# Optimization experiments

Hardware: AMD Instinct MI355X
Metric: run time of the kernel (lower is better)

Reference implementation:

```python
import jax, jax.numpy as jnp
import numpy as np

B, LQ, D, H, L, P, DFF = 16, 1024, 256, 8, 4, 4, 1024
SHAPES = ((64, 64), (32, 32), (16, 16), (8, 8))  # (H_l, W_l) per level
LV = sum(h * w for h, w in SHAPES)  # 5440
DH = D // H
EPS = 1e-5


def layer_norm(x, g, b):
    m = jnp.mean(x, -1, keepdims=True)
    v = jnp.mean((x - m) ** 2, -1, keepdims=True)
    return (x - m) * jax.lax.rsqrt(v + EPS) * g + b


def mha(q_in, k_in, v_in, w, b, ow, ob):
    # torch nn.MultiheadAttention with packed in_proj [3D, D]
    q = (q_in @ w[:D].T + b[:D]).reshape(B, LQ, H, DH)
    k = (k_in @ w[D:2 * D].T + b[D:2 * D]).reshape(B, LQ, H, DH)
    v = (v_in @ w[2 * D:].T + b[2 * D:]).reshape(B, LQ, H, DH)
    a = jax.nn.softmax(jnp.einsum('bqhd,bkhd->bhqk', q, k) * (1.0 / np.sqrt(DH)), -1)
    o = jnp.einsum('bhqk,bkhd->bqhd', a, v).reshape(B, LQ, D)
    return o @ ow.T + ob


def ms_deform_attn(q, ref, src, value_w, value_b, off_w, off_b, attw_w, attw_b, outp_w, outp_b):
    # value: [B, H, LV, DH]
    value = (src @ value_w.T + value_b).reshape(B, LV, H, DH).transpose(0, 2, 1, 3)
    off = (q @ off_w.T + off_b).reshape(B, LQ, H, L, P, 2)
    attw = jax.nn.softmax((q @ attw_w.T + attw_b).reshape(B, LQ, H, L * P), -1).reshape(B, LQ, H, L, P)
    # offset normalizer = (W_l, H_l) matching (x, y) order of reference points
    normalizer = jnp.array([[w, h] for h, w in SHAPES], jnp.float32)
    loc = ref[:, :, None, :, None, :] + off / normalizer[None, None, None, :, None, :]  # [B,LQ,H,L,P,2]
    out = jnp.zeros((B, LQ, H, DH), jnp.float32)
    start = 0
    for l, (hl, wl) in enumerate(SHAPES):
        v = value[:, :, start:start + hl * wl]  # [B,H,N_l,DH]
        start += hl * wl
        # grid_sample semantics, align_corners=False, padding zeros
        x = loc[:, :, :, l, :, 0] * wl - 0.5  # [B,LQ,H,P]
        y = loc[:, :, :, l, :, 1] * hl - 0.5
        x0 = jnp.floor(x); y0 = jnp.floor(y)
        lx = (x - x0).transpose(0, 2, 1, 3)[..., None]  # [B,H,LQ,P,1]
        ly = (y - y0).transpose(0, 2, 1, 3)[..., None]
        x0i = x0.astype(jnp.int32); y0i = y0.astype(jnp.int32)

        def gather(xi, yi):
            valid = ((xi >= 0) & (xi < wl) & (yi >= 0) & (yi < hl)).astype(jnp.float32)
            idx = jnp.clip(yi, 0, hl - 1) * wl + jnp.clip(xi, 0, wl - 1)  # [B,LQ,H,P]
            idx2 = idx.transpose(0, 2, 1, 3).reshape(B, H, LQ * P)
            g = jnp.take_along_axis(v, jnp.broadcast_to(idx2[..., None], (B, H, LQ * P, DH)), axis=2)
            return g.reshape(B, H, LQ, P, DH) * valid.transpose(0, 2, 1, 3)[..., None]

        g00 = gather(x0i, y0i); g01 = gather(x0i + 1, y0i)
        g10 = gather(x0i, y0i + 1); g11 = gather(x0i + 1, y0i + 1)
        sampled = (g00 * (1 - lx) * (1 - ly) + g01 * lx * (1 - ly)
                   + g10 * (1 - lx) * ly + g11 * lx * ly)  # [B,H,LQ,P,DH]
        out = out + jnp.einsum('bhqpd,bqhp->bqhd', sampled, attw[:, :, :, l])
    return out.reshape(B, LQ, D) @ outp_w.T + outp_b


def setup_inputs() -> dict:
    key = jax.random.key(0)
    ks = jax.random.split(key, 16)
    s = 0.02
    inp = {}
    inp['tgt'] = jax.random.normal(ks[0], (B, LQ, D), jnp.float32)
    inp['query_pos'] = jax.random.normal(ks[1], (B, LQ, D), jnp.float32)
    inp['reference_points'] = jax.random.uniform(ks[2], (B, LQ, L, 2), jnp.float32)
    inp['src'] = jax.random.normal(ks[3], (B, LV, D), jnp.float32)
    # self-attention (MHA)
    inp['in_proj_w'] = jax.random.normal(ks[4], (3 * D, D), jnp.float32) * s
    inp['in_proj_b'] = jnp.zeros((3 * D,), jnp.float32)
    inp['out_proj_w'] = jax.random.normal(ks[5], (D, D), jnp.float32) * s
    inp['out_proj_b'] = jnp.zeros((D,), jnp.float32)
    inp['norm2_g'] = jnp.ones((D,), jnp.float32); inp['norm2_b'] = jnp.zeros((D,), jnp.float32)
    # MSDeformAttn
    inp['value_w'] = jax.random.normal(ks[6], (D, D), jnp.float32) * s
    inp['value_b'] = jnp.zeros((D,), jnp.float32)
    inp['off_w'] = jax.random.normal(ks[7], (H * L * P * 2, D), jnp.float32) * s
    inp['off_b'] = jax.random.normal(ks[8], (H * L * P * 2,), jnp.float32) * 0.5
    inp['attw_w'] = jax.random.normal(ks[9], (H * L * P, D), jnp.float32) * s
    inp['attw_b'] = jnp.zeros((H * L * P,), jnp.float32)
    inp['outp_w'] = jax.random.normal(ks[10], (D, D), jnp.float32) * s
    inp['outp_b'] = jnp.zeros((D,), jnp.float32)
    inp['norm1_g'] = jnp.ones((D,), jnp.float32); inp['norm1_b'] = jnp.zeros((D,), jnp.float32)
    # FFN
    inp['lin1_w'] = jax.random.normal(ks[11], (DFF, D), jnp.float32) * s
    inp['lin1_b'] = jnp.zeros((DFF,), jnp.float32)
    inp['lin2_w'] = jax.random.normal(ks[12], (D, DFF), jnp.float32) * s
    inp['lin2_b'] = jnp.zeros((D,), jnp.float32)
    inp['norm3_g'] = jnp.ones((D,), jnp.float32); inp['norm3_b'] = jnp.zeros((D,), jnp.float32)
    inp['src_spatial_shapes'] = jnp.array(SHAPES, jnp.int32)
    inp['level_start_index'] = jnp.array(np.concatenate([[0], np.cumsum([h * w for h, w in SHAPES[:-1]])]), jnp.int32)
    return inp


def reference(tgt, query_pos, reference_points, src,
              in_proj_w, in_proj_b, out_proj_w, out_proj_b, norm2_g, norm2_b,
              value_w, value_b, off_w, off_b, attw_w, attw_b, outp_w, outp_b,
              norm1_g, norm1_b, lin1_w, lin1_b, lin2_w, lin2_b, norm3_g, norm3_b,
              src_spatial_shapes, level_start_index):
    # dropout=0 (eval mode)
    q = tgt + query_pos
    tgt2 = mha(q, q, tgt, in_proj_w, in_proj_b, out_proj_w, out_proj_b)
    tgt = layer_norm(tgt + tgt2, norm2_g, norm2_b)
    tgt2 = ms_deform_attn(tgt + query_pos, reference_points, src,
                          value_w, value_b, off_w, off_b, attw_w, attw_b, outp_w, outp_b)
    tgt = layer_norm(tgt + tgt2, norm1_g, norm1_b)
    t2 = jax.nn.relu(tgt @ lin1_w.T + lin1_b) @ lin2_w.T + lin2_b
    return layer_norm(tgt + t2, norm3_g, norm3_b)
```

## Files before the change

### kernel.cpp

```cpp
#include <hip/hip_runtime.h>
#include <math.h>

typedef short s16x8 __attribute__((ext_vector_type(8)));
typedef float f32x4 __attribute__((ext_vector_type(4)));
typedef unsigned short u16;
typedef unsigned short u16x4 __attribute__((ext_vector_type(4)));
typedef unsigned short u16x8 __attribute__((ext_vector_type(8)));

constexpr int cB    = 16;
constexpr int cLQ   = 1024;
constexpr int cD    = 256;
constexpr int cH    = 8;
constexpr int cLVTOT= 5440;
constexpr int cNTOK = cB * cLQ;
constexpr int cNV   = cB * cLVTOT;

__device__ __forceinline__ u16 f2b(float f) {
    __bf16 h = (__bf16)f;
    u16 u;
    __builtin_memcpy(&u, &h, 2);
    return u;
}
__device__ __forceinline__ float bl(unsigned x) {
    return __uint_as_float(x << 16);
}
__device__ __forceinline__ u16x8 cvt8(float4 a, float4 b) {
    return (u16x8){ f2b(a.x), f2b(a.y), f2b(a.z), f2b(a.w),
                    f2b(b.x), f2b(b.y), f2b(b.z), f2b(b.w) };
}

struct WArgs { const float4* src[8]; };
__global__ __launch_bounds__(256) void prep_all(const float4* __restrict__ t,
                                                const float4* __restrict__ q,
                                                u16x8* __restrict__ tb,
                                                u16x8* __restrict__ qb,
                                                WArgs wa,
                                                u16x8* __restrict__ wout,
                                                const float* __restrict__ off_b,
                                                const float* __restrict__ attw_b,
                                                float* __restrict__ biasoa) {
    int bid = blockIdx.x;
    if (bid < 1024) {
        size_t u = (size_t)bid * 256 + threadIdx.x;
        const float4* tp = t + u * 4;
        const float4* qp = q + u * 4;
        float4 a0 = tp[0], a1 = tp[1], a2 = tp[2], a3 = tp[3];
        float4 b0 = qp[0], b1 = qp[1], b2 = qp[2], b3 = qp[3];
        tb[u * 2]     = cvt8(a0, a1);
        tb[u * 2 + 1] = cvt8(a2, a3);
        float4 s0 = {a0.x + b0.x, a0.y + b0.y, a0.z + b0.z, a0.w + b0.w};
        float4 s1 = {a1.x + b1.x, a1.y + b1.y, a1.z + b1.z, a1.w + b1.w};
        float4 s2 = {a2.x + b2.x, a2.y + b2.y, a2.z + b2.z, a2.w + b2.w};
        float4 s3 = {a3.x + b3.x, a3.y + b3.y, a3.z + b3.z, a3.w + b3.w};
        qb[u * 2]     = cvt8(s0, s1);
        qb[u * 2 + 1] = cvt8(s2, s3);
    } else if (bid < 1272) {
        int u = (bid - 1024) * 256 + threadIdx.x;
        int i = u * 4;
        int s, off;
        if (i < 98304) {
            if (i < 65536) { if (i < 49152) { s = 0; off = i; } else { s = 1; off = i - 49152; } }
            else           { if (i < 81920) { s = 2; off = i - 65536; } else { s = 3; off = i - 81920; } }
        } else {
            if (i < 122880){ if (i < 106496){ s = 4; off = i - 98304; } else { s = 5; off = i - 106496; } }
            else           { if (i < 188416){ s = 6; off = i - 122880; } else { s = 7; off = i - 188416; } }
        }
        const float4* wp = wa.src[s] + off;
        float4 a0 = wp[0], a1 = wp[1], a2 = wp[2], a3 = wp[3];
        wout[(size_t)u * 2]     = cvt8(a0, a1);
        wout[(size_t)u * 2 + 1] = cvt8(a2, a3);
    } else {
        int tix = threadIdx.x;
        biasoa[tix] = off_b[tix];
        if (tix < 128) biasoa[256 + tix] = attw_b[tix];
    }
}

__global__ __launch_bounds__(256) void gemm_qkv_val(const u16* __restrict__ A0,
                                                    const u16* __restrict__ A1,
                                                    const u16* __restrict__ Wt,
                                                    const float* __restrict__ bias,
                                                    u16* __restrict__ QKb,
                                                    u16* __restrict__ Vtg,
                                                    const float* __restrict__ Av,
                                                    const u16* __restrict__ Wv,
                                                    const float* __restrict__ bv,
                                                    u16* __restrict__ Cv) {
    __shared__ u16 As[128 * 32];
    __shared__ u16 Bs[128 * 32];
    const int K = 256;
    int tid = threadIdx.x;
    int bid = blockIdx.x;
    int w = tid >> 6, lane = tid & 63, quad = lane >> 4, l15 = lane & 15;
    int wm = (w & 1) * 64, wn = (w >> 1) * 64;
    int r0 = tid >> 2;
    int c0 = ((tid & 3) ^ ((tid >> 3) & 3)) * 8;
    int abk = (quad ^ ((l15 >> 1) & 3)) * 8;
    f32x4 acc[16];
#pragma unroll
    for (int i = 0; i < 16; ++i) acc[i] = (f32x4){0.f, 0.f, 0.f, 0.f};

    if (bid < 1360) {
        int bm = (bid >> 1) * 128, bn = (bid & 1) * 128;
        const float* ga0 = Av + (size_t)(bm + r0) * 256 + c0;
        const float* ga1 = ga0 + (size_t)64 * 256;
        const u16* gb0 = Wv + (size_t)(bn + r0) * 256 + c0;
        const u16* gb1 = gb0 + (size_t)64 * 256;
        float4 ra0a = *(const float4*)ga0, ra0b = *(const float4*)(ga0 + 4);
        float4 ra1a = *(const float4*)ga1, ra1b = *(const float4*)(ga1 + 4);
        s16x8 rb0 = *(const s16x8*)gb0, rb1 = *(const s16x8*)gb1;
#pragma unroll 2
        for (int i = 0; i < 8; ++i) {
            *(u16x8*)&As[tid * 8]        = cvt8(ra0a, ra0b);
            *(u16x8*)&As[2048 + tid * 8] = cvt8(ra1a, ra1b);
            *(s16x8*)&Bs[tid * 8]        = rb0;
            *(s16x8*)&Bs[2048 + tid * 8] = rb1;
            __syncthreads();
            if (i < 7) {
                int k1 = (i + 1) << 5;
                ra0a = *(const float4*)(ga0 + k1); ra0b = *(const float4*)(ga0 + k1 + 4);
                ra1a = *(const float4*)(ga1 + k1); ra1b = *(const float4*)(ga1 + k1 + 4);
                rb0  = *(const s16x8*)(gb0 + k1);  rb1  = *(const s16x8*)(gb1 + k1);
            }
            s16x8 af[4], bf[4];
#pragma unroll
            for (int mt = 0; mt < 4; ++mt) af[mt] = *(const s16x8*)&As[(wm + mt * 16 + l15) * 32 + abk];
#pragma unroll
            for (int nt = 0; nt < 4; ++nt) bf[nt] = *(const s16x8*)&Bs[(wn + nt * 16 + l15) * 32 + abk];
#pragma unroll
            for (int mt = 0; mt < 4; ++mt)
#pragma unroll
                for (int nt = 0; nt < 4; ++nt)
                    acc[mt * 4 + nt] = __builtin_amdgcn_mfma_f32_16x16x32_bf16(af[mt], bf[nt], acc[mt * 4 + nt], 0, 0, 0);
            __syncthreads();
        }
        float bs[4];
#pragma unroll
        for (int nt = 0; nt < 4; ++nt) bs[nt] = bv[bn + wn + nt * 16 + l15];
#pragma unroll
        for (int mt = 0; mt < 4; ++mt) {
            int m = bm + wm + mt * 16 + quad * 4;
#pragma unroll
            for (int nt = 0; nt < 4; ++nt) {
                int n = bn + wn + nt * 16 + l15;
#pragma unroll
                for (int r = 0; r < 4; ++r)
                    Cv[(size_t)(m + r) * 256 + n] = f2b(acc[mt * 4 + nt][r] + bs[nt]);
            }
        }
        return;
    }
    int id = bid - 1360;
    int bm = (id & 127) * 128;
    int by = id >> 7;
    int bn = by * 128;
    const u16* A = (by < 4) ? A0 : A1;
    const u16* ga0 = A + (size_t)(bm + r0) * K + c0;
    const u16* ga1 = ga0 + (size_t)64 * K;
    const u16* gb0 = Wt + (size_t)(bn + r0) * K + c0;
    const u16* gb1 = gb0 + (size_t)64 * K;
    s16x8 ra0 = *(const s16x8*)ga0, ra1 = *(const s16x8*)ga1;
    s16x8 rb0 = *(const s16x8*)gb0, rb1 = *(const s16x8*)gb1;
#pragma unroll 2
    for (int i = 0; i < 8; ++i) {
        *(s16x8*)&As[tid * 8]        = ra0;
        *(s16x8*)&As[2048 + tid * 8] = ra1;
        *(s16x8*)&Bs[tid * 8]        = rb0;
        *(s16x8*)&Bs[2048 + tid * 8] = rb1;
        __syncthreads();
        if (i < 7) {
            int k1 = (i + 1) << 5;
            ra0 = *(const s16x8*)(ga0 + k1); ra1 = *(const s16x8*)(ga1 + k1);
            rb0 = *(const s16x8*)(gb0 + k1); rb1 = *(const s16x8*)(gb1 + k1);
        }
        s16x8 af[4], bf[4];
#pragma unroll
        for (int mt = 0; mt < 4; ++mt) af[mt] = *(const s16x8*)&As[(wm + mt * 16 + l15) * 32 + abk];
#pragma unroll
        for (int nt = 0; nt < 4; ++nt) bf[nt] = *(const s16x8*)&Bs[(wn + nt * 16 + l15) * 32 + abk];
#pragma unroll
        for (int mt = 0; mt < 4; ++mt)
#pragma unroll
            for (int nt = 0; nt < 4; ++nt)
                acc[mt * 4 + nt] = __builtin_amdgcn_mfma_f32_16x16x32_bf16(af[mt], bf[nt], acc[mt * 4 + nt], 0, 0, 0);
        __syncthreads();
    }
    float bs[4];
#pragma unroll
    for (int nt = 0; nt < 4; ++nt) bs[nt] = bias[bn + wn + nt * 16 + l15];
    if (bn < 512) {
        float qs = (bn + wn < 256) ? 0.25506734f : 1.0f;
#pragma unroll
        for (int mt = 0; mt < 4; ++mt) {
            int m = bm + wm + mt * 16 + quad * 4;
#pragma unroll
            for (int nt = 0; nt < 4; ++nt) {
                int n = bn + wn + nt * 16 + l15;
#pragma unroll
                for (int r = 0; r < 4; ++r)
                    QKb[(size_t)(m + r) * 512 + n] = f2b((acc[mt * 4 + nt][r] + bs[nt]) * qs);
            }
        }
    } else {
#pragma unroll
        for (int mt = 0; mt < 4; ++mt) {
            int m = bm + wm + mt * 16 + quad * 4;
            int b = m >> 10, t = m & 1023;
#pragma unroll
            for (int nt = 0; nt < 4; ++nt) {
                int nv = bn + wn + nt * 16 + l15 - 512;
                int h = nv >> 5, dh = nv & 31;
                u16x4 o;
#pragma unroll
                for (int r = 0; r < 4; ++r) o[r] = f2b(acc[mt * 4 + nt][r] + bs[nt]);
                *(u16x4*)(Vtg + (((size_t)(b * 8 + h) * 32 + dh) << 10) + t) = o;
            }
        }
    }
}

template <int RELU, int OUTBF>
__global__ __launch_bounds__(256) void gemm128(const u16* __restrict__ A,
                                               const u16* __restrict__ Wt,
                                               const float* __restrict__ bias,
                                               float* __restrict__ Cf,
                                               u16* __restrict__ Cb,
                                               int M, int N, int K) {
    __shared__ u16 As[128 * 32];
    __shared__ u16 Bs[128 * 32];
    int tid = threadIdx.x;
    int bm = blockIdx.x * 128, bn = blockIdx.y * 128;
    int w = tid >> 6, lane = tid & 63, quad = lane >> 4, l15 = lane & 15;
    int wm = (w & 1) * 64, wn = (w >> 1) * 64;
    int r0 = tid >> 2;
    int c0 = ((tid & 3) ^ ((tid >> 3) & 3)) * 8;
    const u16* ga0 = A  + (size_t)(bm + r0) * K + c0;
    const u16* ga1 = ga0 + (size_t)64 * K;
    const u16* gb0 = Wt + (size_t)(bn + r0) * K + c0;
    const u16* gb1 = gb0 + (size_t)64 * K;
    int abk = (quad ^ ((l15 >> 1) & 3)) * 8;
    f32x4 acc[16];
#pragma unroll
    for (int i = 0; i < 16; ++i) acc[i] = (f32x4){0.f, 0.f, 0.f, 0.f};
    s16x8 ra0 = *(const s16x8*)ga0, ra1 = *(const s16x8*)ga1;
    s16x8 rb0 = *(const s16x8*)gb0, rb1 = *(const s16x8*)gb1;
    int nk = K >> 5;
#pragma unroll 2
    for (int i = 0; i < nk; ++i) {
        *(s16x8*)&As[tid * 8]        = ra0;
        *(s16x8*)&As[2048 + tid * 8] = ra1;
        *(s16x8*)&Bs[tid * 8]        = rb0;
        *(s16x8*)&Bs[2048 + tid * 8] = rb1;
        __syncthreads();
        if (i + 1 < nk) {
            int k1 = (i + 1) << 5;
            ra0 = *(const s16x8*)(ga0 + k1); ra1 = *(const s16x8*)(ga1 + k1);
            rb0 = *(const s16x8*)(gb0 + k1); rb1 = *(const s16x8*)(gb1 + k1);
        }
        s16x8 af[4], bf[4];
#pragma unroll
        for (int mt = 0; mt < 4; ++mt) af[mt] = *(const s16x8*)&As[(wm + mt * 16 + l15) * 32 + abk];
#pragma unroll
        for (int nt = 0; nt < 4; ++nt) bf[nt] = *(const s16x8*)&Bs[(wn + nt * 16 + l15) * 32 + abk];
#pragma unroll
        for (int mt = 0; mt < 4; ++mt)
#pragma unroll
            for (int nt = 0; nt < 4; ++nt)
                acc[mt * 4 + nt] = __builtin_amdgcn_mfma_f32_16x16x32_bf16(af[mt], bf[nt], acc[mt * 4 + nt], 0, 0, 0);
        __syncthreads();
    }
    float bs[4];
#pragma unroll
    for (int nt = 0; nt < 4; ++nt) bs[nt] = bias[bn + wn + nt * 16 + l15];
#pragma unroll
    for (int mt = 0; mt < 4; ++mt) {
        int m = bm + wm + mt * 16 + quad * 4;
#pragma unroll
        for (int nt = 0; nt < 4; ++nt) {
            int n = bn + wn + nt * 16 + l15;
#pragma unroll
            for (int r = 0; r < 4; ++r) {
                float v = acc[mt * 4 + nt][r] + bs[nt];
                if (RELU) v = fmaxf(v, 0.f);
                if (OUTBF) Cb[(size_t)(m + r) * N + n] = f2b(v);
                else       Cf[(size_t)(m + r) * N + n] = v;
            }
        }
    }
}

template <int RELU, int OUTBF>
__global__ __launch_bounds__(256) void gemm64(const u16* __restrict__ A,
                                              const u16* __restrict__ Wt,
                                              const float* __restrict__ bias,
                                              float* __restrict__ Cf,
                                              u16* __restrict__ Cb,
                                              int M, int N, int K) {
    __shared__ u16 As[64 * 32];
    __shared__ u16 Bs[128 * 32];
    int tid = threadIdx.x;
    int bm = blockIdx.x * 64, bn = blockIdx.y * 128;
    int w = tid >> 6, lane = tid & 63, quad = lane >> 4, l15 = lane & 15;
    int wn = w * 32;
    int r0 = tid >> 2;
    int c0 = ((tid & 3) ^ ((tid >> 3) & 3)) * 8;
    const u16* ga0 = A  + (size_t)(bm + r0) * K + c0;
    const u16* gb0 = Wt + (size_t)(bn + r0) * K + c0;
    const u16* gb1 = gb0 + (size_t)64 * K;
    int abk = (quad ^ ((l15 >> 1) & 3)) * 8;
    f32x4 acc[8];
#pragma unroll
    for (int i = 0; i < 8; ++i) acc[i] = (f32x4){0.f, 0.f, 0.f, 0.f};
    s16x8 ra0 = *(const s16x8*)ga0;
    s16x8 rb0 = *(const s16x8*)gb0, rb1 = *(const s16x8*)gb1;
    int nk = K >> 5;
#pragma unroll 2
    for (int i = 0; i < nk; ++i) {
        *(s16x8*)&As[tid * 8]        = ra0;
        *(s16x8*)&Bs[tid * 8]        = rb0;
        *(s16x8*)&Bs[2048 + tid * 8] = rb1;
        __syncthreads();
        if (i + 1 < nk) {
            int k1 = (i + 1) << 5;
            ra0 = *(const s16x8*)(ga0 + k1);
            rb0 = *(const s16x8*)(gb0 + k1); rb1 = *(const s16x8*)(gb1 + k1);
        }
        s16x8 af[4], bf[2];
#pragma unroll
        for (int mt = 0; mt < 4; ++mt) af[mt] = *(const s16x8*)&As[(mt * 16 + l15) * 32 + abk];
#pragma unroll
        for (int nt = 0; nt < 2; ++nt) bf[nt] = *(const s16x8*)&Bs[(wn + nt * 16 + l15) * 32 + abk];
#pragma unroll
        for (int mt = 0; mt < 4; ++mt)
#pragma unroll
            for (int nt = 0; nt < 2; ++nt)
                acc[mt * 2 + nt] = __builtin_amdgcn_mfma_f32_16x16x32_bf16(af[mt], bf[nt], acc[mt * 2 + nt], 0, 0, 0);
        __syncthreads();
    }
    float bs[2];
#pragma unroll
    for (int nt = 0; nt < 2; ++nt) bs[nt] = bias[bn + wn + nt * 16 + l15];
#pragma unroll
    for (int mt = 0; mt < 4; ++mt) {
        int m = bm + mt * 16 + quad * 4;
#pragma unroll
        for (int nt = 0; nt < 2; ++nt) {
            int n = bn + wn + nt * 16 + l15;
#pragma unroll
            for (int r = 0; r < 4; ++r) {
                float v = acc[mt * 2 + nt][r] + bs[nt];
                if (RELU) v = fmaxf(v, 0.f);
                if (OUTBF) Cb[(size_t)(m + r) * N + n] = f2b(v);
                else       Cf[(size_t)(m + r) * N + n] = v;
            }
        }
    }
}

__global__ __launch_bounds__(256) void attn_sw(const u16* __restrict__ QK,
                                               const u16* __restrict__ Vt,
                                               u16* __restrict__ O) {
    __shared__ __align__(16) u16 smem[8192];
    int tid = threadIdx.x, w = tid >> 6, lane = tid & 63, quad = lane >> 4, l15 = lane & 15;
    u16* Ks  = smem;
    u16* Vs  = smem + 2048;
    u16* Psw = smem + 4096 + w * 1024;
    int id = blockIdx.x;
    int qt = id & 15, bh = id >> 4;
    int h = bh & 7, b = bh >> 3;
    int qbase = qt * 64 + w * 16;
    s16x8 qf = *(const s16x8*)(QK + (size_t)(b * cLQ + qbase + l15) * 512 + h * 32 + quad * 8);
    f32x4 o0 = {0.f,0.f,0.f,0.f}, o1 = {0.f,0.f,0.f,0.f}, o2 = {0.f,0.f,0.f,0.f};
    int skey = tid >> 2, kchunk = tid & 3;
    int ks_off = skey * 32 + ((kchunk ^ ((skey >> 1) & 3)) * 8);
    int sdh = kchunk * 8;
    int vdh = tid >> 3, vchunk = tid & 7;
    int vs_off = vdh * 64 + ((vchunk ^ (vdh & 7)) * 8);
    int vkc = vchunk * 8;
    int ksw = (l15 >> 1) & 3;
    int vsw = l15 & 7;
    size_t kgbase = (size_t)(b * cLQ) * 512 + 256 + h * 32;
    size_t vgbase = (size_t)bh * 32 * cLQ;
    s16x8 kreg = *(const s16x8*)(QK + kgbase + (size_t)skey * 512 + sdh);
    s16x8 vreg = *(const s16x8*)(Vt + vgbase + (size_t)vdh * cLQ + vkc);
    const s16x8 ones = {16256,16256,16256,16256,16256,16256,16256,16256};
    for (int kt = 0; kt < cLQ; kt += 64) {
        __syncthreads();
        *(s16x8*)&Ks[ks_off] = kreg;
        *(s16x8*)&Vs[vs_off] = vreg;
        if (kt + 64 < cLQ) {
            kreg = *(const s16x8*)(QK + kgbase + (size_t)(kt + 64 + skey) * 512 + sdh);
            vreg = *(const s16x8*)(Vt + vgbase + (size_t)vdh * cLQ + kt + 64 + vkc);
        }
        __syncthreads();
#pragma unroll
        for (int t = 0; t < 4; ++t) {
            s16x8 kf = *(const s16x8*)&Ks[(t * 16 + l15) * 32 + (quad ^ ksw) * 8];
            f32x4 z = {0.f,0.f,0.f,0.f};
            f32x4 sc = __builtin_amdgcn_mfma_f32_16x16x32_bf16(kf, qf, z, 0, 0, 0);
            u16x4 pb;
#pragma unroll
            for (int r = 0; r < 4; ++r) pb[r] = f2b(exp2f(sc[r]));
            *(u16x4*)&Psw[l15 * 64 + (((t * 2 + (quad >> 1)) ^ vsw) * 8) + (quad & 1) * 4] = pb;
        }
#pragma unroll
        for (int ks = 0; ks < 2; ++ks) {
            int coff = ((ks * 4 + quad) ^ vsw) * 8;
            s16x8 pa  = *(const s16x8*)&Psw[l15 * 64 + coff];
            s16x8 vb0 = *(const s16x8*)&Vs[l15 * 64 + coff];
            s16x8 vb1 = *(const s16x8*)&Vs[(l15 + 16) * 64 + coff];
            o0 = __builtin_amdgcn_mfma_f32_16x16x32_bf16(pa, vb0, o0, 0, 0, 0);
            o1 = __builtin_amdgcn_mfma_f32_16x16x32_bf16(pa, vb1, o1, 0, 0, 0);
            o2 = __builtin_amdgcn_mfma_f32_16x16x32_bf16(pa, ones, o2, 0, 0, 0);
        }
    }
#pragma unroll
    for (int r = 0; r < 4; ++r) {
        float inv = 1.0f / o2[r];
        int q = qbase + quad * 4 + r;
        size_t ob = (size_t)(b * cLQ + q) * cD + h * 32;
        O[ob + l15]      = f2b(o0[r] * inv);
        O[ob + 16 + l15] = f2b(o1[r] * inv);
    }
}

template <int WB, int QP>
__global__ __launch_bounds__(256) void add_ln_kernel(const float* __restrict__ X,
                                                     const float* __restrict__ R,
                                                     const float* __restrict__ g,
                                                     const float* __restrict__ bt,
                                                     const float* __restrict__ qp,
                                                     float* __restrict__ out,
                                                     u16* __restrict__ outb) {
    int wave = threadIdx.x / 64;
    int lane = threadIdx.x % 64;
    int row = blockIdx.x * 4 + wave;
    const float* x = X + (size_t)row * cD;
    const float* r = R + (size_t)row * cD;
    float4 xv = *(const float4*)(x + lane * 4);
    float4 rv = *(const float4*)(r + lane * 4);
    float v0 = xv.x + rv.x, v1 = xv.y + rv.y, v2 = xv.z + rv.z, v3 = xv.w + rv.w;
    float s = v0 + v1 + v2 + v3;
    float s2 = v0 * v0 + v1 * v1 + v2 * v2 + v3 * v3;
#pragma unroll
    for (int off = 32; off > 0; off >>= 1) {
        s += __shfl_xor(s, off);
        s2 += __shfl_xor(s2, off);
    }
    float mean = s * (1.0f / 256.0f);
    float var = s2 * (1.0f / 256.0f) - mean * mean;
    float rstd = rsqrtf(var + 1e-5f);
    float4 gv = *(const float4*)(g + lane * 4);
    float4 bv = *(const float4*)(bt + lane * 4);
    float4 o;
    o.x = (v0 - mean) * rstd * gv.x + bv.x;
    o.y = (v1 - mean) * rstd * gv.y + bv.y;
    o.z = (v2 - mean) * rstd * gv.z + bv.z;
    o.w = (v3 - mean) * rstd * gv.w + bv.w;
    *(float4*)(out + (size_t)row * cD + lane * 4) = o;
    if (WB) {
        u16x4 ob = { f2b(o.x), f2b(o.y), f2b(o.z), f2b(o.w) };
        *(u16x4*)(outb + (size_t)row * cD + lane * 4) = ob;
    }
    if (QP) {
        float4 qv = *(const float4*)(qp + (size_t)row * cD + lane * 4);
        u16x4 ob = { f2b(o.x + qv.x), f2b(o.y + qv.y), f2b(o.z + qv.z), f2b(o.w + qv.w) };
        *(u16x4*)(outb + (size_t)row * cD + lane * 4) = ob;
    }
}

__global__ __launch_bounds__(256) void deform_kernel(const u16* __restrict__ value,
                                                     const float* __restrict__ oa,
                                                     const float* __restrict__ refp,
                                                     u16* __restrict__ out) {
    int t = blockIdx.x * 32 + (threadIdx.x >> 3);
    int dq = threadIdx.x & 7;
    int h = t & 7;
    int bq = t >> 3;
    int b = bq >> 10;
    const float* al = oa + (size_t)bq * 384 + 256 + h * 16;
    float wv[16];
    float mx = -1e30f;
#pragma unroll
    for (int i = 0; i < 16; ++i) { wv[i] = al[i]; mx = fmaxf(mx, wv[i]); }
    float sum = 0.f;
#pragma unroll
    for (int i = 0; i < 16; ++i) { wv[i] = __expf(wv[i] - mx); sum += wv[i]; }
    float inv = 1.f / sum;
    const float* off = oa + (size_t)bq * 384 + h * 32;
    const float* rp = refp + (size_t)bq * 8;
    float wgtA[4], wgtB[4];
    int   idxA[4], idxB[4];
#pragma unroll
    for (int k = 0; k < 2; ++k) {
        int s = dq * 2 + k;
        int l = s >> 2;
        int dim = 64 >> l;
        unsigned start = (16384u - (16384u >> (2 * l))) / 3u;
        float ox = off[s * 2 + 0];
        float oy = off[s * 2 + 1];
        float x = rp[l * 2 + 0] * (float)dim + ox - 0.5f;
        float y = rp[l * 2 + 1] * (float)dim + oy - 0.5f;
        float x0f = floorf(x), y0f = floorf(y);
        float lx = x - x0f, ly = y - y0f;
        int x0 = (int)x0f, y0 = (int)y0f;
        float aw = wv[s] * inv;
        float cw[4] = {(1.f - lx) * (1.f - ly), lx * (1.f - ly),
                       (1.f - lx) * ly, lx * ly};
        int xs[4] = {x0, x0 + 1, x0, x0 + 1};
        int ys[4] = {y0, y0, y0 + 1, y0 + 1};
#pragma unroll
        for (int c = 0; c < 4; ++c) {
            int xi = xs[c], yi = ys[c];
            bool valid = (xi >= 0) && (xi < dim) && (yi >= 0) && (yi < dim);
            int xc = min(max(xi, 0), dim - 1);
            int yc = min(max(yi, 0), dim - 1);
            int ix = (int)start + yc * dim + xc;
            float wg = valid ? aw * cw[c] : 0.f;
            if (k == 0) { wgtA[c] = wg; idxA[c] = ix; }
            else        { wgtB[c] = wg; idxB[c] = ix; }
        }
    }
    const u16* vb = value + ((size_t)b * cLVTOT) * 256 + h * 32 + dq * 4;
    float a0 = 0.f, a1 = 0.f, a2 = 0.f, a3 = 0.f;
#pragma unroll
    for (int s = 0; s < 16; ++s) {
        int srcl = s >> 1;
#pragma unroll
        for (int c = 0; c < 4; ++c) {
            float wgt = __shfl((s & 1) ? wgtB[c] : wgtA[c], srcl, 8);
            int   idx = __shfl((s & 1) ? idxB[c] : idxA[c], srcl, 8);
            unsigned long long u = *(const unsigned long long*)(vb + (size_t)idx * 256);
            a0 += wgt * bl((unsigned)(u & 0xffffull));
            a1 += wgt * bl((unsigned)((u >> 16) & 0xffffull));
            a2 += wgt * bl((unsigned)((u >> 32) & 0xffffull));
            a3 += wgt * bl((unsigned)(u >> 48));
        }
    }
    u16x4 o = { f2b(a0), f2b(a1), f2b(a2), f2b(a3) };
    *(u16x4*)(out + (size_t)bq * 256 + h * 32 + dq * 4) = o;
}

extern "C" void kernel_launch(void* const* d_in, const int* in_sizes, int n_in,
                              void* d_out, int out_size, void* d_ws, size_t ws_size,
                              hipStream_t stream) {
    const float* tgt        = (const float*)d_in[0];
    const float* query_pos  = (const float*)d_in[1];
    const float* refp       = (const float*)d_in[2];
    const float* src        = (const float*)d_in[3];
    const float* in_proj_w  = (const float*)d_in[4];
    const float* in_proj_b  = (const float*)d_in[5];
    const float* out_proj_b = (const float*)d_in[7];
    const float* norm2_g    = (const float*)d_in[8];
    const float* norm2_b    = (const float*)d_in[9];
    const float* value_b    = (const float*)d_in[11];
    const float* off_b      = (const float*)d_in[13];
    const float* attw_b     = (const float*)d_in[15];
    const float* outp_b     = (const float*)d_in[17];
    const float* norm1_g    = (const float*)d_in[18];
    const float* norm1_b    = (const float*)d_in[19];
    const float* lin1_b     = (const float*)d_in[21];
    const float* lin2_b     = (const float*)d_in[23];
    const float* norm3_g    = (const float*)d_in[24];
    const float* norm3_b    = (const float*)d_in[25];

    char* W = (char*)d_ws;
    const size_t S84 = 8388608;
    u16*   tgtb  = (u16*)(W + 0);
    u16*   q2b   = (u16*)(W + 0);
    u16*   qb    = (u16*)(W + 1 * S84);
    u16*   QKb   = (u16*)(W + 2 * S84);
    u16*   dtb   = (u16*)(W + 2 * S84);
    u16*   x2b   = (u16*)(W + 3 * S84);
    float* ffn2f = (float*)(W + 4 * S84);
    u16*   aob   = (u16*)(W + 5 * S84);
    float* oaf   = (float*)(W + 5 * S84);
    u16*   Vtg   = (u16*)(W + 6 * S84);
    float* t2f   = (float*)(W + 6 * S84);
    float* x1f   = (float*)(W + 8 * S84);
    float* x2f   = (float*)(W + 10 * S84);
    u16*   ffn1b = (u16*)(W + 12 * S84);
    u16*   valb  = (u16*)(W + 12 * S84 + 44564480);
    char*  wbase = W + 12 * S84 + 2 * 44564480;
    u16* wb_in   = (u16*)(wbase + 0);
    u16* wb_out  = (u16*)(wbase + 393216);
    u16* wb_val  = (u16*)(wbase + 524288);
    u16* wb_off  = (u16*)(wbase + 655360);
    u16* wb_outp = (u16*)(wbase + 851968);
    u16* wb_lin1 = (u16*)(wbase + 983040);
    u16* wb_lin2 = (u16*)(wbase + 1507328);
    float* biasoa= (float*)(wbase + 2031616);
    float* out = (float*)d_out;

    dim3 blk(256);

    WArgs wa;
    wa.src[0] = (const float4*)in_proj_w;  wa.src[1] = (const float4*)d_in[6];
    wa.src[2] = (const float4*)d_in[10];   wa.src[3] = (const float4*)d_in[12];
    wa.src[4] = (const float4*)d_in[14];   wa.src[5] = (const float4*)d_in[16];
    wa.src[6] = (const float4*)d_in[20];   wa.src[7] = (const float4*)d_in[22];
    prep_all<<<dim3(1273), blk, 0, stream>>>((const float4*)tgt, (const float4*)query_pos,
                                             (u16x8*)tgtb, (u16x8*)qb,
                                             wa, (u16x8*)wb_in, off_b, attw_b, biasoa);

    gemm_qkv_val<<<dim3(2128), blk, 0, stream>>>(qb, tgtb, wb_in, in_proj_b, QKb, Vtg,
                                                 src, wb_val, value_b, valb);
    attn_sw<<<dim3(cB * cH * 16), blk, 0, stream>>>(QKb, Vtg, aob);
    gemm64<0, 0><<<dim3(256, 2), blk, 0, stream>>>(aob, wb_out, out_proj_b, t2f, nullptr, cNTOK, 256, 256);
    add_ln_kernel<0, 1><<<dim3(4096), blk, 0, stream>>>(tgt, t2f, norm2_g, norm2_b, query_pos, x1f, q2b);

    gemm64<0, 0><<<dim3(256, 3), blk, 0, stream>>>(q2b, wb_off, biasoa, oaf, nullptr, cNTOK, 384, 256);
    deform_kernel<<<dim3(4096), blk, 0, stream>>>(valb, oaf, refp, dtb);
    gemm64<0, 0><<<dim3(256, 2), blk, 0, stream>>>(dtb, wb_outp, outp_b, t2f, nullptr, cNTOK, 256, 256);
    add_ln_kernel<1, 0><<<dim3(4096), blk, 0, stream>>>(x1f, t2f, norm1_g, norm1_b, nullptr, x2f, x2b);

    gemm128<1, 1><<<dim3(128, 8), blk, 0, stream>>>(x2b, wb_lin1, lin1_b, nullptr, ffn1b, cNTOK, 1024, 256);
    gemm64<0, 0><<<dim3(256, 2), blk, 0, stream>>>(ffn1b, wb_lin2, lin2_b, ffn2f, nullptr, cNTOK, 256, 1024);
    add_ln_kernel<0, 0><<<dim3(4096), blk, 0, stream>>>(x2f, ffn2f, norm3_g, norm3_b, nullptr, out, nullptr);
}
```

Baseline: 425.6 us.

## Fuse tgt+query_pos bf16 conversion into QKV GEMM and split value GEMM

```diff
diff --git a/kernel.cpp b/kernel.cpp
--- a/kernel.cpp
+++ b/kernel.cpp
@@ -30,147 +30,91 @@
 }
 
 struct WArgs { const float4* src[8]; };
-__global__ __launch_bounds__(256) void prep_all(const float4* __restrict__ t,
-                                                const float4* __restrict__ q,
-                                                u16x8* __restrict__ tb,
-                                                u16x8* __restrict__ qb,
-                                                WArgs wa,
-                                                u16x8* __restrict__ wout,
-                                                const float* __restrict__ off_b,
-                                                const float* __restrict__ attw_b,
-                                                float* __restrict__ biasoa) {
+__global__ __launch_bounds__(256) void prep_w(WArgs wa,
+                                              u16x8* __restrict__ wout,
+                                              const float* __restrict__ off_b,
+                                              const float* __restrict__ attw_b,
+                                              float* __restrict__ biasoa) {
     int bid = blockIdx.x;
-    if (bid < 1024) {
-        size_t u = (size_t)bid * 256 + threadIdx.x;
-        const float4* tp = t + u * 4;
-        const float4* qp = q + u * 4;
-        float4 a0 = tp[0], a1 = tp[1], a2 = tp[2], a3 = tp[3];
-        float4 b0 = qp[0], b1 = qp[1], b2 = qp[2], b3 = qp[3];
-        tb[u * 2]     = cvt8(a0, a1);
-        tb[u * 2 + 1] = cvt8(a2, a3);
-        float4 s0 = {a0.x + b0.x, a0.y + b0.y, a0.z + b0.z, a0.w + b0.w};
-        float4 s1 = {a1.x + b1.x, a1.y + b1.y, a1.z + b1.z, a1.w + b1.w};
-        float4 s2 = {a2.x + b2.x, a2.y + b2.y, a2.z + b2.z, a2.w + b2.w};
-        float4 s3 = {a3.x + b3.x, a3.y + b3.y, a3.z + b3.z, a3.w + b3.w};
-        qb[u * 2]     = cvt8(s0, s1);
-        qb[u * 2 + 1] = cvt8(s2, s3);
-    } else if (bid < 1272) {
-        int u = (bid - 1024) * 256 + threadIdx.x;
-        int i = u * 4;
-        int s, off;
-        if (i < 98304) {
-            if (i < 65536) { if (i < 49152) { s = 0; off = i; } else { s = 1; off = i - 49152; } }
-            else           { if (i < 81920) { s = 2; off = i - 65536; } else { s = 3; off = i - 81920; } }
-        } else {
-            if (i < 122880){ if (i < 106496){ s = 4; off = i - 98304; } else { s = 5; off = i - 106496; } }
-            else           { if (i < 188416){ s = 6; off = i - 122880; } else { s = 7; off = i - 188416; } }
-        }
-        const float4* wp = wa.src[s] + off;
-        float4 a0 = wp[0], a1 = wp[1], a2 = wp[2], a3 = wp[3];
-        wout[(size_t)u * 2]     = cvt8(a0, a1);
-        wout[(size_t)u * 2 + 1] = cvt8(a2, a3);
-    } else {
+    if (bid >= 248) {
         int tix = threadIdx.x;
         biasoa[tix] = off_b[tix];
         if (tix < 128) biasoa[256 + tix] = attw_b[tix];
-    }
-}
-
-__global__ __launch_bounds__(256) void gemm_qkv_val(const u16* __restrict__ A0,
-                                                    const u16* __restrict__ A1,
+        return;
+    }
+    int u = bid * 256 + threadIdx.x;
+    int i = u * 4;
+    int s, off;
+    if (i < 98304) {
+        if (i < 65536) { if (i < 49152) { s = 0; off = i; } else { s = 1; off = i - 49152; } }
+        else           { if (i < 81920) { s = 2; off = i - 65536; } else { s = 3; off = i - 81920; } }
+    } else {
+        if (i < 122880){ if (i < 106496){ s = 4; off = i - 98304; } else { s = 5; off = i - 106496; } }
+        else           { if (i < 188416){ s = 6; off = i - 122880; } else { s = 7; off = i - 188416; } }
+    }
+    const float4* wp = wa.src[s] + off;
+    float4 a0 = wp[0], a1 = wp[1], a2 = wp[2], a3 = wp[3];
+    wout[(size_t)u * 2]     = cvt8(a0, a1);
+    wout[(size_t)u * 2 + 1] = cvt8(a2, a3);
+}
+
+__global__ __launch_bounds__(256) void gemm_qkv_f32(const float* __restrict__ T,
+                                                    const float* __restrict__ P,
                                                     const u16* __restrict__ Wt,
                                                     const float* __restrict__ bias,
                                                     u16* __restrict__ QKb,
-                                                    u16* __restrict__ Vtg,
-                                                    const float* __restrict__ Av,
-                                                    const u16* __restrict__ Wv,
-                                                    const float* __restrict__ bv,
-                                                    u16* __restrict__ Cv) {
+                                                    u16* __restrict__ Vtg) {
     __shared__ u16 As[128 * 32];
     __shared__ u16 Bs[128 * 32];
-    const int K = 256;
-    int tid = threadIdx.x;
-    int bid = blockIdx.x;
+    int tid = threadIdx.x, bid = blockIdx.x;
     int w = tid >> 6, lane = tid & 63, quad = lane >> 4, l15 = lane & 15;
     int wm = (w & 1) * 64, wn = (w >> 1) * 64;
+    int bm = (bid & 127) * 128;
+    int by = bid >> 7;
+    int bn = by * 128;
+    bool addq = by < 4;
     int r0 = tid >> 2;
     int c0 = ((tid & 3) ^ ((tid >> 3) & 3)) * 8;
+    const float* gt0 = T + (size_t)(bm + r0) * 256 + c0;
+    const float* gt1 = gt0 + (size_t)64 * 256;
+    const float* gp0 = P + (size_t)(bm + r0) * 256 + c0;
+    const float* gp1 = gp0 + (size_t)64 * 256;
+    const u16* gb0 = Wt + (size_t)(bn + r0) * 256 + c0;
+    const u16* gb1 = gb0 + (size_t)64 * 256;
     int abk = (quad ^ ((l15 >> 1) & 3)) * 8;
     f32x4 acc[16];
 #pragma unroll
     for (int i = 0; i < 16; ++i) acc[i] = (f32x4){0.f, 0.f, 0.f, 0.f};
-
-    if (bid < 1360) {
-        int bm = (bid >> 1) * 128, bn = (bid & 1) * 128;
-        const float* ga0 = Av + (size_t)(bm + r0) * 256 + c0;
-        const float* ga1 = ga0 + (size_t)64 * 256;
-        const u16* gb0 = Wv + (size_t)(bn + r0) * 256 + c0;
-        const u16* gb1 = gb0 + (size_t)64 * 256;
-        float4 ra0a = *(const float4*)ga0, ra0b = *(const float4*)(ga0 + 4);
-        float4 ra1a = *(const float4*)ga1, ra1b = *(const float4*)(ga1 + 4);
-        s16x8 rb0 = *(const s16x8*)gb0, rb1 = *(const s16x8*)gb1;
-#pragma unroll 2
-        for (int i = 0; i < 8; ++i) {
-            *(u16x8*)&As[tid * 8]        = cvt8(ra0a, ra0b);
-            *(u16x8*)&As[2048 + tid * 8] = cvt8(ra1a, ra1b);
-            *(s16x8*)&Bs[tid * 8]        = rb0;
-            *(s16x8*)&Bs[2048 + tid * 8] = rb1;
-            __syncthreads();
-            if (i < 7) {
-                int k1 = (i + 1) << 5;
-                ra0a = *(const float4*)(ga0 + k1); ra0b = *(const float4*)(ga0 + k1 + 4);
-                ra1a = *(const float4*)(ga1 + k1); ra1b = *(const float4*)(ga1 + k1 + 4);
-                rb0  = *(const s16x8*)(gb0 + k1);  rb1  = *(const s16x8*)(gb1 + k1);
-            }
-            s16x8 af[4], bf[4];
-#pragma unroll
-            for (int mt = 0; mt < 4; ++mt) af[mt] = *(const s16x8*)&As[(wm + mt * 16 + l15) * 32 + abk];
-#pragma unroll
-            for (int nt = 0; nt < 4; ++nt) bf[nt] = *(const s16x8*)&Bs[(wn + nt * 16 + l15) * 32 + abk];
-#pragma unroll
-            for (int mt = 0; mt < 4; ++mt)
-#pragma unroll
-                for (int nt = 0; nt < 4; ++nt)
-                    acc[mt * 4 + nt] = __builtin_amdgcn_mfma_f32_16x16x32_bf16(af[mt], bf[nt], acc[mt * 4 + nt], 0, 0, 0);
-            __syncthreads();
-        }
-        float bs[4];
-#pragma unroll
-        for (int nt = 0; nt < 4; ++nt) bs[nt] = bv[bn + wn + nt * 16 + l15];
-#pragma unroll
-        for (int mt = 0; mt < 4; ++mt) {
-            int m = bm + wm + mt * 16 + quad * 4;
-#pragma unroll
-            for (int nt = 0; nt < 4; ++nt) {
-                int n = bn + wn + nt * 16 + l15;
-#pragma unroll
-                for (int r = 0; r < 4; ++r)
-                    Cv[(size_t)(m + r) * 256 + n] = f2b(acc[mt * 4 + nt][r] + bs[nt]);
-            }
-        }
-        return;
-    }
-    int id = bid - 1360;
-    int bm = (id & 127) * 128;
-    int by = id >> 7;
-    int bn = by * 128;
-    const u16* A = (by < 4) ? A0 : A1;
-    const u16* ga0 = A + (size_t)(bm + r0) * K + c0;
-    const u16* ga1 = ga0 + (size_t)64 * K;
-    const u16* gb0 = Wt + (size_t)(bn + r0) * K + c0;
-    const u16* gb1 = gb0 + (size_t)64 * K;
-    s16x8 ra0 = *(const s16x8*)ga0, ra1 = *(const s16x8*)ga1;
+    float4 t0a = *(const float4*)gt0, t0b = *(const float4*)(gt0 + 4);
+    float4 t1a = *(const float4*)gt1, t1b = *(const float4*)(gt1 + 4);
+    float4 p0a, p0b, p1a, p1b;
+    if (addq) {
+        p0a = *(const float4*)gp0; p0b = *(const float4*)(gp0 + 4);
+        p1a = *(const float4*)gp1; p1b = *(const float4*)(gp1 + 4);
+    }
     s16x8 rb0 = *(const s16x8*)gb0, rb1 = *(const s16x8*)gb1;
 #pragma unroll 2
     for (int i = 0; i < 8; ++i) {
-        *(s16x8*)&As[tid * 8]        = ra0;
-        *(s16x8*)&As[2048 + tid * 8] = ra1;
+        float4 s0a = t0a, s0b = t0b, s1a = t1a, s1b = t1b;
+        if (addq) {
+            s0a.x += p0a.x; s0a.y += p0a.y; s0a.z += p0a.z; s0a.w += p0a.w;
+            s0b.x += p0b.x; s0b.y += p0b.y; s0b.z += p0b.z; s0b.w += p0b.w;
+            s1a.x += p1a.x; s1a.y += p1a.y; s1a.z += p1a.z; s1a.w += p1a.w;
+            s1b.x += p1b.x; s1b.y += p1b.y; s1b.z += p1b.z; s1b.w += p1b.w;
+        }
+        *(u16x8*)&As[tid * 8]        = cvt8(s0a, s0b);
+        *(u16x8*)&As[2048 + tid * 8] = cvt8(s1a, s1b);
         *(s16x8*)&Bs[tid * 8]        = rb0;
         *(s16x8*)&Bs[2048 + tid * 8] = rb1;
         __syncthreads();
         if (i < 7) {
             int k1 = (i + 1) << 5;
-            ra0 = *(const s16x8*)(ga0 + k1); ra1 = *(const s16x8*)(ga1 + k1);
+            t0a = *(const float4*)(gt0 + k1); t0b = *(const float4*)(gt0 + k1 + 4);
+            t1a = *(const float4*)(gt1 + k1); t1b = *(const float4*)(gt1 + k1 + 4);
+            if (addq) {
+                p0a = *(const float4*)(gp0 + k1); p0b = *(const float4*)(gp0 + k1 + 4);
+                p1a = *(const float4*)(gp1 + k1); p1b = *(const float4*)(gp1 + k1 + 4);
+            }
             rb0 = *(const s16x8*)(gb0 + k1); rb1 = *(const s16x8*)(gb1 + k1);
         }
         s16x8 af[4], bf[4];
@@ -215,6 +159,70 @@
                 for (int r = 0; r < 4; ++r) o[r] = f2b(acc[mt * 4 + nt][r] + bs[nt]);
                 *(u16x4*)(Vtg + (((size_t)(b * 8 + h) * 32 + dh) << 10) + t) = o;
             }
+        }
+    }
+}
+
+__global__ __launch_bounds__(256) void gemm_val(const float* __restrict__ Av,
+                                                const u16* __restrict__ Wv,
+                                                const float* __restrict__ bv,
+                                                u16* __restrict__ Cv) {
+    __shared__ u16 As[128 * 32];
+    __shared__ u16 Bs[128 * 32];
+    int tid = threadIdx.x, bid = blockIdx.x;
+    int w = tid >> 6, lane = tid & 63, quad = lane >> 4, l15 = lane & 15;
+    int wm = (w & 1) * 64, wn = (w >> 1) * 64;
+    int bm = (bid >> 1) * 128, bn = (bid & 1) * 128;
+    int r0 = tid >> 2;
+    int c0 = ((tid & 3) ^ ((tid >> 3) & 3)) * 8;
+    const float* ga0 = Av + (size_t)(bm + r0) * 256 + c0;
+    const float* ga1 = ga0 + (size_t)64 * 256;
+    const u16* gb0 = Wv + (size_t)(bn + r0) * 256 + c0;
+    const u16* gb1 = gb0 + (size_t)64 * 256;
+    int abk = (quad ^ ((l15 >> 1) & 3)) * 8;
+    f32x4 acc[16];
+#pragma unroll
+    for (int i = 0; i < 16; ++i) acc[i] = (f32x4){0.f, 0.f, 0.f, 0.f};
+    float4 ra0a = *(const float4*)ga0, ra0b = *(const float4*)(ga0 + 4);
+    float4 ra1a = *(const float4*)ga1, ra1b = *(const float4*)(ga1 + 4);
+    s16x8 rb0 = *(const s16x8*)gb0, rb1 = *(const s16x8*)gb1;
+#pragma unroll 2
+    for (int i = 0; i < 8; ++i) {
+        *(u16x8*)&As[tid * 8]        = cvt8(ra0a, ra0b);
+        *(u16x8*)&As[2048 + tid * 8] = cvt8(ra1a, ra1b);
+        *(s16x8*)&Bs[tid * 8]        = rb0;
+        *(s16x8*)&Bs[2048 + tid * 8] = rb1;
+        __syncthreads();
+        if (i < 7) {
+            int k1 = (i + 1) << 5;
+            ra0a = *(const float4*)(ga0 + k1); ra0b = *(const float4*)(ga0 + k1 + 4);
+            ra1a = *(const float4*)(ga1 + k1); ra1b = *(const float4*)(ga1 + k1 + 4);
+            rb0  = *(const s16x8*)(gb0 + k1);  rb1  = *(const s16x8*)(gb1 + k1);
+        }
+        s16x8 af[4], bf[4];
+#pragma unroll
+        for (int mt = 0; mt < 4; ++mt) af[mt] = *(const s16x8*)&As[(wm + mt * 16 + l15) * 32 + abk];
+#pragma unroll
+        for (int nt = 0; nt < 4; ++nt) bf[nt] = *(const s16x8*)&Bs[(wn + nt * 16 + l15) * 32 + abk];
+#pragma unroll
+        for (int mt = 0; mt < 4; ++mt)
+#pragma unroll
+            for (int nt = 0; nt < 4; ++nt)
+                acc[mt * 4 + nt] = __builtin_amdgcn_mfma_f32_16x16x32_bf16(af[mt], bf[nt], acc[mt * 4 + nt], 0, 0, 0);
+        __syncthreads();
+    }
+    float bs[4];
+#pragma unroll
+    for (int nt = 0; nt < 4; ++nt) bs[nt] = bv[bn + wn + nt * 16 + l15];
+#pragma unroll
+    for (int mt = 0; mt < 4; ++mt) {
+        int m = bm + wm + mt * 16 + quad * 4;
+#pragma unroll
+        for (int nt = 0; nt < 4; ++nt) {
+            int n = bn + wn + nt * 16 + l15;
+#pragma unroll
+            for (int r = 0; r < 4; ++r)
+                Cv[(size_t)(m + r) * 256 + n] = f2b(acc[mt * 4 + nt][r] + bs[nt]);
         }
     }
 }
@@ -366,7 +374,8 @@
     u16* Vs  = smem + 2048;
     u16* Psw = smem + 4096 + w * 1024;
     int id = blockIdx.x;
-    int qt = id & 15, bh = id >> 4;
+    int xcd = id & 7, qt = (id >> 3) & 15;
+    int bh = (id >> 7) * 8 + xcd;
     int h = bh & 7, b = bh >> 3;
     int qbase = qt * 64 + w * 16;
     s16x8 qf = *(const s16x8*)(QK + (size_t)(b * cLQ + qbase + l15) * 512 + h * 32 + quad * 8);
@@ -566,9 +575,7 @@
 
     char* W = (char*)d_ws;
     const size_t S84 = 8388608;
-    u16*   tgtb  = (u16*)(W + 0);
     u16*   q2b   = (u16*)(W + 0);
-    u16*   qb    = (u16*)(W + 1 * S84);
     u16*   QKb   = (u16*)(W + 2 * S84);
     u16*   dtb   = (u16*)(W + 2 * S84);
     u16*   x2b   = (u16*)(W + 3 * S84);
@@ -599,13 +606,11 @@
     wa.src[2] = (const float4*)d_in[10];   wa.src[3] = (const float4*)d_in[12];
     wa.src[4] = (const float4*)d_in[14];   wa.src[5] = (const float4*)d_in[16];
     wa.src[6] = (const float4*)d_in[20];   wa.src[7] = (const float4*)d_in[22];
-    prep_all<<<dim3(1273), blk, 0, stream>>>((const float4*)tgt, (const float4*)query_pos,
-                                             (u16x8*)tgtb, (u16x8*)qb,
-                                             wa, (u16x8*)wb_in, off_b, attw_b, biasoa);
-
-    gemm_qkv_val<<<dim3(2128), blk, 0, stream>>>(qb, tgtb, wb_in, in_proj_b, QKb, Vtg,
-                                                 src, wb_val, value_b, valb);
+    prep_w<<<dim3(249), blk, 0, stream>>>(wa, (u16x8*)wb_in, off_b, attw_b, biasoa);
+
+    gemm_qkv_f32<<<dim3(768), blk, 0, stream>>>(tgt, query_pos, wb_in, in_proj_b, QKb, Vtg);
     attn_sw<<<dim3(cB * cH * 16), blk, 0, stream>>>(QKb, Vtg, aob);
+    gemm_val<<<dim3(1360), blk, 0, stream>>>(src, wb_val, value_b, valb);
     gemm64<0, 0><<<dim3(256, 2), blk, 0, stream>>>(aob, wb_out, out_proj_b, t2f, nullptr, cNTOK, 256, 256);
     add_ln_kernel<0, 1><<<dim3(4096), blk, 0, stream>>>(tgt, t2f, norm2_g, norm2_b, query_pos, x1f, q2b);
 
```

Measured after the change: 431.3 us. Within noise of the previous version (+1.3%).
